# Kernel tuning notes

Hardware: AMD Instinct MI355X
Metric: run time of the kernel (lower is better)

Reference implementation:

```python
import jax, jax.numpy as jnp
from jax import lax
import numpy as np

B, T, I, H, L, C = 256, 128, 512, 512, 5, 40

def setup_inputs() -> dict:
    key = jax.random.key(0)
    ks = jax.random.split(key, 8)
    s = 1.0 / np.sqrt(H)
    u = lambda k, shape: jax.random.uniform(k, shape, jnp.float32, -s, s)
    x = jax.random.normal(ks[0], (B, T, I), jnp.float32)
    Wih = u(ks[1], (L, 4 * H, I))   # layer input->gates (I==H so uniform stack)
    Whh = u(ks[2], (L, 4 * H, H))
    bih = u(ks[3], (L, 4 * H))
    bhh = u(ks[4], (L, 4 * H))
    Wfc = u(ks[5], (C, H))
    bfc = u(ks[6], (C,))
    return {"x": x, "Wih": Wih, "Whh": Whh, "bih": bih, "bhh": bhh, "Wfc": Wfc, "bfc": bfc}

def _lstm_layer(x, Wih, Whh, bih, bhh):
    # Precompute input contribution for all timesteps: [B,T,4H]
    xw = jnp.einsum('bti,gi->btg', x, Wih) + bih + bhh
    Bn = x.shape[0]
    init = (jnp.zeros((Bn, H), x.dtype), jnp.zeros((Bn, H), x.dtype))
    def step(carry, xw_t):
        h, c = carry
        g = xw_t + h @ Whh.T
        i, f, gg, o = jnp.split(g, 4, axis=-1)  # PyTorch gate order i,f,g,o
        c = jax.nn.sigmoid(f) * c + jax.nn.sigmoid(i) * jnp.tanh(gg)
        h = jax.nn.sigmoid(o) * jnp.tanh(c)
        return (h, c), h
    _, hs = lax.scan(step, init, jnp.swapaxes(xw, 0, 1))  # hs: [T,B,H]
    return jnp.swapaxes(hs, 0, 1)

def reference(x, Wih, Whh, bih, bhh, Wfc, bfc):
    h = x
    for l in range(L):
        h = _lstm_layer(h, Wih[l], Whh[l], bih[l], bhh[l])
    return h[:, -1, :] @ Wfc.T + bfc  # [B, C]
```

## Files before the change

### kernel.cpp

```cpp
#include <hip/hip_runtime.h>

typedef _Float16 f16x8 __attribute__((ext_vector_type(8)));
typedef float f32x4 __attribute__((ext_vector_type(4)));

static constexpr int NL = 5;
static constexpr int NBATCH = 256;
static constexpr int NT = 128;
static constexpr int NH = 512;
static constexpr int NG = 2048;
static constexpr int NC = 40;

__global__ void f32_to_f16_kernel(const float* __restrict__ src,
                                  _Float16* __restrict__ dst, int n) {
  int i = blockIdx.x * blockDim.x + threadIdx.x;
  int stride = gridDim.x * blockDim.x;
  for (; i < n; i += stride) dst[i] = (_Float16)src[i];
}

__global__ __launch_bounds__(256) void lstm_slot_kernel(
    const _Float16* __restrict__ wih_h, const _Float16* __restrict__ whh_h,
    const _Float16* __restrict__ x_h, const float* __restrict__ bih,
    const float* __restrict__ bhh, _Float16* __restrict__ h_xfer,
    float* __restrict__ c_state, int s) {
  const int bid = blockIdx.x;
  const int mb = bid / 80;
  const int rem = bid - mb * 80;
  const int layer = rem >> 4;
  const int nb = rem & 15;
  const int t = s - layer;
  if (t < 0 || t >= NT) return;

  const int tid = threadIdx.x;
  const int wv = tid >> 6;
  const int lane = tid & 63;
  const int lrow = lane & 15;
  const int lk = (lane >> 4) << 3;
  const int m0 = mb * 64;
  const int u0 = nb * 32;

  const _Float16* aptr;
  size_t astride;
  if (layer == 0) {
    aptr = x_h + (size_t)t * NH;
    astride = (size_t)NT * NH;
  } else {
    aptr = h_xfer + (size_t)((layer - 1) * 2 + (t & 1)) * NBATCH * NH;
    astride = NH;
  }

  const _Float16* wih = wih_h + (size_t)layer * NG * NH;
  const _Float16* whh = whh_h + (size_t)layer * NG * NH;
  const int ncol = wv * NH + u0 + lrow;

  f32x4 acc[4][2];
#pragma unroll
  for (int i = 0; i < 4; ++i)
#pragma unroll
    for (int j = 0; j < 2; ++j) acc[i][j] = (f32x4){0.f, 0.f, 0.f, 0.f};

  {
    const _Float16* arow = aptr + (size_t)(m0 + lrow) * astride + lk;
    const _Float16* brow = wih + (size_t)ncol * NH + lk;
#pragma unroll 2
    for (int kk = 0; kk < 16; ++kk) {
      const int kc = kk << 5;
      f16x8 a0 = *(const f16x8*)(arow + kc);
      f16x8 a1 = *(const f16x8*)(arow + 16 * astride + kc);
      f16x8 a2 = *(const f16x8*)(arow + 32 * astride + kc);
      f16x8 a3 = *(const f16x8*)(arow + 48 * astride + kc);
      f16x8 b0 = *(const f16x8*)(brow + kc);
      f16x8 b1 = *(const f16x8*)(brow + 16 * NH + kc);
      acc[0][0] = __builtin_amdgcn_mfma_f32_16x16x32_f16(a0, b0, acc[0][0], 0, 0, 0);
      acc[1][0] = __builtin_amdgcn_mfma_f32_16x16x32_f16(a1, b0, acc[1][0], 0, 0, 0);
      acc[2][0] = __builtin_amdgcn_mfma_f32_16x16x32_f16(a2, b0, acc[2][0], 0, 0, 0);
      acc[3][0] = __builtin_amdgcn_mfma_f32_16x16x32_f16(a3, b0, acc[3][0], 0, 0, 0);
      acc[0][1] = __builtin_amdgcn_mfma_f32_16x16x32_f16(a0, b1, acc[0][1], 0, 0, 0);
      acc[1][1] = __builtin_amdgcn_mfma_f32_16x16x32_f16(a1, b1, acc[1][1], 0, 0, 0);
      acc[2][1] = __builtin_amdgcn_mfma_f32_16x16x32_f16(a2, b1, acc[2][1], 0, 0, 0);
      acc[3][1] = __builtin_amdgcn_mfma_f32_16x16x32_f16(a3, b1, acc[3][1], 0, 0, 0);
    }
  }

  if (t > 0) {
    const _Float16* hp =
        h_xfer + (size_t)(layer * 2 + ((t + 1) & 1)) * NBATCH * NH;
    const _Float16* arow = hp + (size_t)(m0 + lrow) * NH + lk;
    const _Float16* brow = whh + (size_t)ncol * NH + lk;
#pragma unroll 2
    for (int kk = 0; kk < 16; ++kk) {
      const int kc = kk << 5;
      f16x8 a0 = *(const f16x8*)(arow + kc);
      f16x8 a1 = *(const f16x8*)(arow + 16 * NH + kc);
      f16x8 a2 = *(const f16x8*)(arow + 32 * NH + kc);
      f16x8 a3 = *(const f16x8*)(arow + 48 * NH + kc);
      f16x8 b0 = *(const f16x8*)(brow + kc);
      f16x8 b1 = *(const f16x8*)(brow + 16 * NH + kc);
      acc[0][0] = __builtin_amdgcn_mfma_f32_16x16x32_f16(a0, b0, acc[0][0], 0, 0, 0);
      acc[1][0] = __builtin_amdgcn_mfma_f32_16x16x32_f16(a1, b0, acc[1][0], 0, 0, 0);
      acc[2][0] = __builtin_amdgcn_mfma_f32_16x16x32_f16(a2, b0, acc[2][0], 0, 0, 0);
      acc[3][0] = __builtin_amdgcn_mfma_f32_16x16x32_f16(a3, b0, acc[3][0], 0, 0, 0);
      acc[0][1] = __builtin_amdgcn_mfma_f32_16x16x32_f16(a0, b1, acc[0][1], 0, 0, 0);
      acc[1][1] = __builtin_amdgcn_mfma_f32_16x16x32_f16(a1, b1, acc[1][1], 0, 0, 0);
      acc[2][1] = __builtin_amdgcn_mfma_f32_16x16x32_f16(a2, b1, acc[2][1], 0, 0, 0);
      acc[3][1] = __builtin_amdgcn_mfma_f32_16x16x32_f16(a3, b1, acc[3][1], 0, 0, 0);
    }
  }

  __shared__ float gsm[64][132];
  const int r0 = (lane >> 4) << 2;
#pragma unroll
  for (int mt = 0; mt < 4; ++mt)
#pragma unroll
    for (int nt = 0; nt < 2; ++nt) {
#pragma unroll
      for (int r = 0; r < 4; ++r)
        gsm[mt * 16 + r0 + r][(wv << 5) + (nt << 4) + lrow] = acc[mt][nt][r];
    }
  __syncthreads();

  const int ml = tid >> 2;
  const int uq = (tid & 3) << 3;
  const int b = m0 + ml;
  const float* bi = bih + layer * NG;
  const float* bh = bhh + layer * NG;
  float* cs = c_state + ((size_t)layer * NBATCH + b) * NH;
  _Float16* hout =
      h_xfer + ((size_t)(layer * 2 + (t & 1)) * NBATCH + b) * NH;
#pragma unroll
  for (int j = 0; j < 8; ++j) {
    const int ul = uq + j;
    const int u = u0 + ul;
    float gi = gsm[ml][ul] + bi[u] + bh[u];
    float gf = gsm[ml][32 + ul] + bi[NH + u] + bh[NH + u];
    float gg = gsm[ml][64 + ul] + bi[2 * NH + u] + bh[2 * NH + u];
    float go = gsm[ml][96 + ul] + bi[3 * NH + u] + bh[3 * NH + u];
    float cp = (t == 0) ? 0.f : cs[u];
    float is = 1.f / (1.f + __expf(-gi));
    float fs = 1.f / (1.f + __expf(-gf));
    float gt = 2.f / (1.f + __expf(-2.f * gg)) - 1.f;
    float os = 1.f / (1.f + __expf(-go));
    float c = fs * cp + is * gt;
    cs[u] = c;
    float th = 2.f / (1.f + __expf(-2.f * c)) - 1.f;
    hout[u] = (_Float16)(os * th);
  }
}

__global__ __launch_bounds__(64) void fc_kernel(
    const _Float16* __restrict__ h_xfer, const float* __restrict__ wfc,
    const float* __restrict__ bfc, float* __restrict__ out) {
  const _Float16* h = h_xfer + (size_t)(4 * 2 + 1) * NBATCH * NH;
  const int b = blockIdx.x;
  const int lane = threadIdx.x;
  __shared__ float hrow[NH];
  for (int k = lane; k < NH; k += 64) hrow[k] = (float)h[(size_t)b * NH + k];
  __syncthreads();
  if (lane < NC) {
    const float* w = wfc + (size_t)lane * NH;
    float acc = bfc[lane];
#pragma unroll 8
    for (int k = 0; k < NH; ++k) acc += hrow[k] * w[k];
    out[b * NC + lane] = acc;
  }
}

extern "C" void kernel_launch(void* const* d_in, const int* in_sizes, int n_in,
                              void* d_out, int out_size, void* d_ws,
                              size_t ws_size, hipStream_t stream) {
  const float* x = (const float*)d_in[0];
  const float* Wih = (const float*)d_in[1];
  const float* Whh = (const float*)d_in[2];
  const float* bih = (const float*)d_in[3];
  const float* bhh = (const float*)d_in[4];
  const float* Wfc = (const float*)d_in[5];
  const float* bfc = (const float*)d_in[6];
  float* out = (float*)d_out;

  char* ws = (char*)d_ws;
  size_t off = 0;
  _Float16* wih_h = (_Float16*)(ws + off); off += (size_t)NL * NG * NH * 2;
  _Float16* whh_h = (_Float16*)(ws + off); off += (size_t)NL * NG * NH * 2;
  _Float16* x_h   = (_Float16*)(ws + off); off += (size_t)NBATCH * NT * NH * 2;
  _Float16* h_xfer = (_Float16*)(ws + off); off += (size_t)NL * 2 * NBATCH * NH * 2;
  float* c_st = (float*)(ws + off); off += (size_t)NL * NBATCH * NH * 4;

  f32_to_f16_kernel<<<1024, 256, 0, stream>>>(Wih, wih_h, NL * NG * NH);
  f32_to_f16_kernel<<<1024, 256, 0, stream>>>(Whh, whh_h, NL * NG * NH);
  f32_to_f16_kernel<<<2048, 256, 0, stream>>>(x, x_h, NBATCH * NT * NH);

  for (int s = 0; s < NT + NL - 1; ++s)
    lstm_slot_kernel<<<320, 256, 0, stream>>>(wih_h, whh_h, x_h, bih, bhh,
                                              h_xfer, c_st, s);

  fc_kernel<<<NBATCH, 64, 0, stream>>>(h_xfer, Wfc, bfc, out);
}
```

Before: 6.897 ms.

## Replace per-step LSTM launches with a persistent kernel holding weights in LDS

Replaces the 132 per-timestep launches with a single persistent kernel of 160 blocks, one per (layer, 16-unit slice). Each block converts its Wih/Whh rows to fp16 once and keeps them swizzled in 128KB of dynamic LDS. Blocks synchronise between wavefront steps with a global atomic-counter barrier. The cell state stays in registers, and the gate combination uses lane shuffles instead of a shared-memory transpose. This removes launch overhead, repeated weight reloads and the separate weight-conversion kernels. In exchange, correctness depends on all 160 blocks being co-resident, and a spin barrier now runs at every step.

```diff
diff --git a/kernel.cpp b/kernel.cpp
--- a/kernel.cpp
+++ b/kernel.cpp
@@ -9,6 +9,8 @@
 static constexpr int NH = 512;
 static constexpr int NG = 2048;
 static constexpr int NC = 40;
+static constexpr int NBLK = 160;
+static constexpr int PLANE = NBATCH * NH;
 
 __global__ void f32_to_f16_kernel(const float* __restrict__ src,
                                   _Float16* __restrict__ dst, int n) {
@@ -17,139 +19,162 @@
   for (; i < n; i += stride) dst[i] = (_Float16)src[i];
 }
 
-__global__ __launch_bounds__(256) void lstm_slot_kernel(
-    const _Float16* __restrict__ wih_h, const _Float16* __restrict__ whh_h,
+__global__ __launch_bounds__(512, 2) void lstm_persist(
+    const float* __restrict__ Wih, const float* __restrict__ Whh,
     const _Float16* __restrict__ x_h, const float* __restrict__ bih,
     const float* __restrict__ bhh, _Float16* __restrict__ h_xfer,
-    float* __restrict__ c_state, int s) {
+    unsigned* __restrict__ bar_cnt) {
+  extern __shared__ _Float16 wlds[];
+
   const int bid = blockIdx.x;
-  const int mb = bid / 80;
-  const int rem = bid - mb * 80;
-  const int layer = rem >> 4;
-  const int nb = rem & 15;
-  const int t = s - layer;
-  if (t < 0 || t >= NT) return;
-
+  const int layer = bid >> 5;
+  const int nb = bid & 31;
   const int tid = threadIdx.x;
+  const int lane = tid & 63;
   const int wv = tid >> 6;
-  const int lane = tid & 63;
+  const int mq = wv >> 1;
+  const int nq = wv & 1;
   const int lrow = lane & 15;
   const int lk = (lane >> 4) << 3;
-  const int m0 = mb * 64;
-  const int u0 = nb * 32;
-
-  const _Float16* aptr;
-  size_t astride;
-  if (layer == 0) {
-    aptr = x_h + (size_t)t * NH;
-    astride = (size_t)NT * NH;
-  } else {
-    aptr = h_xfer + (size_t)((layer - 1) * 2 + (t & 1)) * NBATCH * NH;
-    astride = NH;
-  }
-
-  const _Float16* wih = wih_h + (size_t)layer * NG * NH;
-  const _Float16* whh = whh_h + (size_t)layer * NG * NH;
-  const int ncol = wv * NH + u0 + lrow;
-
-  f32x4 acc[4][2];
-#pragma unroll
-  for (int i = 0; i < 4; ++i)
-#pragma unroll
-    for (int j = 0; j < 2; ++j) acc[i][j] = (f32x4){0.f, 0.f, 0.f, 0.f};
+  const int swz = (lane & 7) << 4;
+  const int m0 = mq * 64;
 
   {
-    const _Float16* arow = aptr + (size_t)(m0 + lrow) * astride + lk;
-    const _Float16* brow = wih + (size_t)ncol * NH + lk;
+    const float* wi = Wih + (size_t)layer * NG * NH;
+    const float* wh = Whh + (size_t)layer * NG * NH;
+    for (int c = tid; c < 64 * 128; c += 512) {
+      const int wrow = c >> 7;
+      const int k16 = c & 127;
+      const int g = wrow >> 4, j = wrow & 15;
+      const size_t grow = (size_t)(g * NH + nb * 16 + j) * NH;
+      const float* src =
+          (k16 < 64) ? (wi + grow + k16 * 8) : (wh + grow + (k16 - 64) * 8);
+      f16x8 v;
+#pragma unroll
+      for (int e = 0; e < 8; ++e) v[e] = (_Float16)src[e];
+      const int boff = wrow * 2048 + ((k16 * 16) ^ ((wrow & 7) << 4));
+      *(f16x8*)((char*)wlds + boff) = v;
+    }
+  }
+
+  for (int i = bid * 512 + tid; i < NL * PLANE; i += NBLK * 512) {
+    const int l = i >> 17;
+    const int off = i & (PLANE - 1);
+    h_xfer[(size_t)(l * 2 + 1) * PLANE + off] = (_Float16)0.f;
+  }
+
+  const int u_loc = nq * 8 + (lane & 7);
+  const int u = nb * 16 + u_loc;
+  const float bs0 = bih[layer * NG + 0 * NH + u] + bhh[layer * NG + 0 * NH + u];
+  const float bs1 = bih[layer * NG + 1 * NH + u] + bhh[layer * NG + 1 * NH + u];
+  const float bs2 = bih[layer * NG + 2 * NH + u] + bhh[layer * NG + 2 * NH + u];
+  const float bs3 = bih[layer * NG + 3 * NH + u] + bhh[layer * NG + 3 * NH + u];
+
+  const int wrow0 = ((lrow >> 3) + 0) * 16 + u_loc;
+  const int wrow1 = ((lrow >> 3) + 2) * 16 + u_loc;
+  const int wb0 = wrow0 * 2048;
+  const int wb1 = wrow1 * 2048;
+
+  float cst[8];
+#pragma unroll
+  for (int i = 0; i < 8; ++i) cst[i] = 0.f;
+
+  __syncthreads();
+
+  for (int s = 0; s < NT + NL - 1; ++s) {
+    const int t = s - layer;
+    if (t >= 0 && t < NT) {
+      f32x4 acc[4][2];
+#pragma unroll
+      for (int i = 0; i < 4; ++i)
+#pragma unroll
+        for (int j = 0; j < 2; ++j) acc[i][j] = (f32x4){0.f, 0.f, 0.f, 0.f};
+
+      auto do_half = [&](const _Float16* aptr, size_t astr, int kbase) {
+        const _Float16* ar = aptr + (size_t)(m0 + lrow) * astr + lk;
 #pragma unroll 2
-    for (int kk = 0; kk < 16; ++kk) {
-      const int kc = kk << 5;
-      f16x8 a0 = *(const f16x8*)(arow + kc);
-      f16x8 a1 = *(const f16x8*)(arow + 16 * astride + kc);
-      f16x8 a2 = *(const f16x8*)(arow + 32 * astride + kc);
-      f16x8 a3 = *(const f16x8*)(arow + 48 * astride + kc);
-      f16x8 b0 = *(const f16x8*)(brow + kc);
-      f16x8 b1 = *(const f16x8*)(brow + 16 * NH + kc);
-      acc[0][0] = __builtin_amdgcn_mfma_f32_16x16x32_f16(a0, b0, acc[0][0], 0, 0, 0);
-      acc[1][0] = __builtin_amdgcn_mfma_f32_16x16x32_f16(a1, b0, acc[1][0], 0, 0, 0);
-      acc[2][0] = __builtin_amdgcn_mfma_f32_16x16x32_f16(a2, b0, acc[2][0], 0, 0, 0);
-      acc[3][0] = __builtin_amdgcn_mfma_f32_16x16x32_f16(a3, b0, acc[3][0], 0, 0, 0);
-      acc[0][1] = __builtin_amdgcn_mfma_f32_16x16x32_f16(a0, b1, acc[0][1], 0, 0, 0);
-      acc[1][1] = __builtin_amdgcn_mfma_f32_16x16x32_f16(a1, b1, acc[1][1], 0, 0, 0);
-      acc[2][1] = __builtin_amdgcn_mfma_f32_16x16x32_f16(a2, b1, acc[2][1], 0, 0, 0);
-      acc[3][1] = __builtin_amdgcn_mfma_f32_16x16x32_f16(a3, b1, acc[3][1], 0, 0, 0);
+        for (int kk = 0; kk < 16; ++kk) {
+          const int kc = kk << 5;
+          f16x8 a0 = *(const f16x8*)(ar + kc);
+          f16x8 a1 = *(const f16x8*)(ar + 16 * astr + kc);
+          f16x8 a2 = *(const f16x8*)(ar + 32 * astr + kc);
+          f16x8 a3 = *(const f16x8*)(ar + 48 * astr + kc);
+          const int ko = ((lk + kc + kbase) << 1) ^ swz;
+          f16x8 b0 = *(const f16x8*)((const char*)wlds + wb0 + ko);
+          f16x8 b1 = *(const f16x8*)((const char*)wlds + wb1 + ko);
+          acc[0][0] = __builtin_amdgcn_mfma_f32_16x16x32_f16(a0, b0, acc[0][0], 0, 0, 0);
+          acc[1][0] = __builtin_amdgcn_mfma_f32_16x16x32_f16(a1, b0, acc[1][0], 0, 0, 0);
+          acc[2][0] = __builtin_amdgcn_mfma_f32_16x16x32_f16(a2, b0, acc[2][0], 0, 0, 0);
+          acc[3][0] = __builtin_amdgcn_mfma_f32_16x16x32_f16(a3, b0, acc[3][0], 0, 0, 0);
+          acc[0][1] = __builtin_amdgcn_mfma_f32_16x16x32_f16(a0, b1, acc[0][1], 0, 0, 0);
+          acc[1][1] = __builtin_amdgcn_mfma_f32_16x16x32_f16(a1, b1, acc[1][1], 0, 0, 0);
+          acc[2][1] = __builtin_amdgcn_mfma_f32_16x16x32_f16(a2, b1, acc[2][1], 0, 0, 0);
+          acc[3][1] = __builtin_amdgcn_mfma_f32_16x16x32_f16(a3, b1, acc[3][1], 0, 0, 0);
+        }
+      };
+
+      if (layer == 0) {
+        do_half(x_h + (size_t)t * NH, (size_t)NT * NH, 0);
+      } else {
+        do_half(h_xfer + (size_t)((layer - 1) * 2 + (t & 1)) * PLANE,
+                (size_t)NH, 0);
+      }
+      if (t > 0) {
+        do_half(h_xfer + (size_t)(layer * 2 + ((t - 1) & 1)) * PLANE,
+                (size_t)NH, 512);
+      }
+
+      _Float16* hout = h_xfer + (size_t)(layer * 2 + (t & 1)) * PLANE;
+      const int rbase = (lane & 8) ? 2 : 0;
+#pragma unroll
+      for (int mt = 0; mt < 4; ++mt) {
+#pragma unroll
+        for (int rr = 0; rr < 2; ++rr) {
+          float own0 = acc[mt][0][rbase + rr];
+          float own1 = acc[mt][1][rbase + rr];
+          float snd0 = (lane & 8) ? acc[mt][0][rr] : acc[mt][0][2 + rr];
+          float snd1 = (lane & 8) ? acc[mt][1][rr] : acc[mt][1][2 + rr];
+          float rcv0 = __shfl_xor(snd0, 8);
+          float rcv1 = __shfl_xor(snd1, 8);
+          float gi = ((lane & 8) ? rcv0 : own0) + bs0;
+          float gf = ((lane & 8) ? own0 : rcv0) + bs1;
+          float gg = ((lane & 8) ? rcv1 : own1) + bs2;
+          float go = ((lane & 8) ? own1 : rcv1) + bs3;
+          float cp = cst[mt * 2 + rr];
+          float is = 1.f / (1.f + __expf(-gi));
+          float fs = 1.f / (1.f + __expf(-gf));
+          float gt = 2.f / (1.f + __expf(-2.f * gg)) - 1.f;
+          float os = 1.f / (1.f + __expf(-go));
+          float c = fs * cp + is * gt;
+          cst[mt * 2 + rr] = c;
+          float th = 2.f / (1.f + __expf(-2.f * c)) - 1.f;
+          const int row = m0 + mt * 16 + ((lane >> 4) << 2) + rbase + rr;
+          hout[(size_t)row * NH + u] = (_Float16)(os * th);
+        }
+      }
     }
-  }
-
-  if (t > 0) {
-    const _Float16* hp =
-        h_xfer + (size_t)(layer * 2 + ((t + 1) & 1)) * NBATCH * NH;
-    const _Float16* arow = hp + (size_t)(m0 + lrow) * NH + lk;
-    const _Float16* brow = whh + (size_t)ncol * NH + lk;
-#pragma unroll 2
-    for (int kk = 0; kk < 16; ++kk) {
-      const int kc = kk << 5;
-      f16x8 a0 = *(const f16x8*)(arow + kc);
-      f16x8 a1 = *(const f16x8*)(arow + 16 * NH + kc);
-      f16x8 a2 = *(const f16x8*)(arow + 32 * NH + kc);
-      f16x8 a3 = *(const f16x8*)(arow + 48 * NH + kc);
-      f16x8 b0 = *(const f16x8*)(brow + kc);
-      f16x8 b1 = *(const f16x8*)(brow + 16 * NH + kc);
-      acc[0][0] = __builtin_amdgcn_mfma_f32_16x16x32_f16(a0, b0, acc[0][0], 0, 0, 0);
-      acc[1][0] = __builtin_amdgcn_mfma_f32_16x16x32_f16(a1, b0, acc[1][0], 0, 0, 0);
-      acc[2][0] = __builtin_amdgcn_mfma_f32_16x16x32_f16(a2, b0, acc[2][0], 0, 0, 0);
-      acc[3][0] = __builtin_amdgcn_mfma_f32_16x16x32_f16(a3, b0, acc[3][0], 0, 0, 0);
-      acc[0][1] = __builtin_amdgcn_mfma_f32_16x16x32_f16(a0, b1, acc[0][1], 0, 0, 0);
-      acc[1][1] = __builtin_amdgcn_mfma_f32_16x16x32_f16(a1, b1, acc[1][1], 0, 0, 0);
-      acc[2][1] = __builtin_amdgcn_mfma_f32_16x16x32_f16(a2, b1, acc[2][1], 0, 0, 0);
-      acc[3][1] = __builtin_amdgcn_mfma_f32_16x16x32_f16(a3, b1, acc[3][1], 0, 0, 0);
+
+    __threadfence();
+    __syncthreads();
+    if (tid == 0) {
+      atomicAdd(bar_cnt, 1u);
+      const unsigned tgt = (unsigned)(s + 1) * NBLK;
+      int guard = 0;
+      while (__hip_atomic_load(bar_cnt, __ATOMIC_RELAXED,
+                               __HIP_MEMORY_SCOPE_AGENT) < tgt) {
+        __builtin_amdgcn_s_sleep(2);
+        if (++guard > 200000000) break;
+      }
     }
-  }
-
-  __shared__ float gsm[64][132];
-  const int r0 = (lane >> 4) << 2;
-#pragma unroll
-  for (int mt = 0; mt < 4; ++mt)
-#pragma unroll
-    for (int nt = 0; nt < 2; ++nt) {
-#pragma unroll
-      for (int r = 0; r < 4; ++r)
-        gsm[mt * 16 + r0 + r][(wv << 5) + (nt << 4) + lrow] = acc[mt][nt][r];
-    }
-  __syncthreads();
-
-  const int ml = tid >> 2;
-  const int uq = (tid & 3) << 3;
-  const int b = m0 + ml;
-  const float* bi = bih + layer * NG;
-  const float* bh = bhh + layer * NG;
-  float* cs = c_state + ((size_t)layer * NBATCH + b) * NH;
-  _Float16* hout =
-      h_xfer + ((size_t)(layer * 2 + (t & 1)) * NBATCH + b) * NH;
-#pragma unroll
-  for (int j = 0; j < 8; ++j) {
-    const int ul = uq + j;
-    const int u = u0 + ul;
-    float gi = gsm[ml][ul] + bi[u] + bh[u];
-    float gf = gsm[ml][32 + ul] + bi[NH + u] + bh[NH + u];
-    float gg = gsm[ml][64 + ul] + bi[2 * NH + u] + bh[2 * NH + u];
-    float go = gsm[ml][96 + ul] + bi[3 * NH + u] + bh[3 * NH + u];
-    float cp = (t == 0) ? 0.f : cs[u];
-    float is = 1.f / (1.f + __expf(-gi));
-    float fs = 1.f / (1.f + __expf(-gf));
-    float gt = 2.f / (1.f + __expf(-2.f * gg)) - 1.f;
-    float os = 1.f / (1.f + __expf(-go));
-    float c = fs * cp + is * gt;
-    cs[u] = c;
-    float th = 2.f / (1.f + __expf(-2.f * c)) - 1.f;
-    hout[u] = (_Float16)(os * th);
+    __syncthreads();
+    __threadfence();
   }
 }
 
 __global__ __launch_bounds__(64) void fc_kernel(
     const _Float16* __restrict__ h_xfer, const float* __restrict__ wfc,
     const float* __restrict__ bfc, float* __restrict__ out) {
-  const _Float16* h = h_xfer + (size_t)(4 * 2 + 1) * NBATCH * NH;
+  const _Float16* h = h_xfer + (size_t)(4 * 2 + 1) * PLANE;
   const int b = blockIdx.x;
   const int lane = threadIdx.x;
   __shared__ float hrow[NH];
@@ -178,19 +203,22 @@
 
   char* ws = (char*)d_ws;
   size_t off = 0;
-  _Float16* wih_h = (_Float16*)(ws + off); off += (size_t)NL * NG * NH * 2;
-  _Float16* whh_h = (_Float16*)(ws + off); off += (size_t)NL * NG * NH * 2;
-  _Float16* x_h   = (_Float16*)(ws + off); off += (size_t)NBATCH * NT * NH * 2;
-  _Float16* h_xfer = (_Float16*)(ws + off); off += (size_t)NL * 2 * NBATCH * NH * 2;
-  float* c_st = (float*)(ws + off); off += (size_t)NL * NBATCH * NH * 4;
-
-  f32_to_f16_kernel<<<1024, 256, 0, stream>>>(Wih, wih_h, NL * NG * NH);
-  f32_to_f16_kernel<<<1024, 256, 0, stream>>>(Whh, whh_h, NL * NG * NH);
+  _Float16* x_h = (_Float16*)(ws + off);
+  off += (size_t)NBATCH * NT * NH * 2;
+  _Float16* h_xfer = (_Float16*)(ws + off);
+  off += (size_t)NL * 2 * PLANE * 2;
+  off = (off + 255) & ~(size_t)255;
+  unsigned* bar_cnt = (unsigned*)(ws + off);
+  off += 256;
+
+  hipFuncSetAttribute((const void*)lstm_persist,
+                      hipFuncAttributeMaxDynamicSharedMemorySize, 131072);
+
   f32_to_f16_kernel<<<2048, 256, 0, stream>>>(x, x_h, NBATCH * NT * NH);
-
-  for (int s = 0; s < NT + NL - 1; ++s)
-    lstm_slot_kernel<<<320, 256, 0, stream>>>(wih_h, whh_h, x_h, bih, bhh,
-                                              h_xfer, c_st, s);
+  hipMemsetAsync(bar_cnt, 0, 256, stream);
+
+  lstm_persist<<<NBLK, 512, 131072, stream>>>(Wih, Whh, x_h, bih, bhh, h_xfer,
+                                              bar_cnt);
 
   fc_kernel<<<NBATCH, 64, 0, stream>>>(h_xfer, Wfc, bfc, out);
 }
```

New measurement: 13.05 ms. +89.3%, slower.
